# Kernel tuning notes

Hardware: AMD Instinct MI355X
Metric: run time of the kernel (lower is better)

## Reference

```python
import jax, jax.numpy as jnp
import numpy as np

N_NODES = 40000
N_EDGES = 640000
D = 128
BN_EPS = 1e-5


def setup_inputs() -> dict:
    key = jax.random.key(0)
    ks = jax.random.split(key, 8)
    h = jax.random.normal(ks[0], (N_NODES, D), dtype=jnp.float32)
    snorm_n = jax.random.uniform(ks[1], (N_NODES, 1), dtype=jnp.float32)
    W_self = jax.random.normal(ks[2], (D, D), dtype=jnp.float32) * 0.05
    W_neigh = jax.random.normal(ks[3], (D, D), dtype=jnp.float32) * 0.05
    b = jax.random.normal(ks[4], (D,), dtype=jnp.float32) * 0.05
    gamma = jnp.ones((D,), dtype=jnp.float32)
    beta = jnp.zeros((D,), dtype=jnp.float32)
    src = jax.random.randint(ks[5], (N_EDGES,), 0, N_NODES, dtype=jnp.int32)
    dst = jax.random.randint(ks[6], (N_EDGES,), 0, N_NODES, dtype=jnp.int32)
    return {"h": h, "snorm_n": snorm_n, "W_self": W_self, "W_neigh": W_neigh,
            "b": b, "gamma": gamma, "beta": beta, "src": src, "dst": dst}


def reference(h, snorm_n, W_self, W_neigh, b, gamma, beta, src, dst):
    h_in = h
    # --- SAGEConv (mean aggregator): mean over in-neighbors (src -> dst) ---
    msg = h[src]                                   # [E, D] irregular gather
    agg = jax.ops.segment_sum(msg, dst, num_segments=N_NODES)  # [N, D]
    deg = jax.ops.segment_sum(jnp.ones((N_EDGES,), h.dtype), dst,
                              num_segments=N_NODES)            # [N]
    h_neigh = agg / jnp.maximum(deg, 1.0)[:, None]
    out = h @ W_self + h_neigh @ W_neigh + b       # fc_self + fc_neigh + bias
    out = jax.nn.relu(out)                         # activation
    # --- graph norm ---
    out = out * snorm_n
    # --- batch norm (training-style batch statistics over nodes) ---
    mean = jnp.mean(out, axis=0)
    var = jnp.var(out, axis=0)
    out = (out - mean) * jax.lax.rsqrt(var + BN_EPS) * gamma + beta
    # --- residual ---
    return h_in + out
```

## Files before the change

kernel.cpp:

```cpp
#include <hip/hip_runtime.h>
#include <hip/hip_bf16.h>

constexpr int N_NODES = 40000;
constexpr int N_EDGES = 640000;
constexpr int D = 128;
constexpr float BN_EPS = 1e-5f;
constexpr int SCAN_BLOCKS = 157;

typedef __attribute__((ext_vector_type(8))) short short8;
typedef __attribute__((ext_vector_type(4))) float f32x4;

static_assert(N_EDGES == N_NODES * D / 8, "hist_cvt fusion assumes equal ranges");

__device__ __forceinline__ unsigned bf16_rne(float f) {
    unsigned b = __float_as_uint(f);
    return (b + 0x7FFFu + ((b >> 16) & 1u)) >> 16;
}
__device__ __forceinline__ float bflo(unsigned w) { return __uint_as_float(w << 16); }
__device__ __forceinline__ float bfhi(unsigned w) { return __uint_as_float(w & 0xFFFF0000u); }

__global__ void hist_cvt_kernel(const int* __restrict__ dst,
                                int* __restrict__ deg_i,
                                const float4* __restrict__ h4,
                                uint4* __restrict__ hb4,
                                const float* __restrict__ Wself,
                                const float* __restrict__ Wneigh,
                                uint4* __restrict__ wfrag) {
    int e = blockIdx.x * blockDim.x + threadIdx.x;
    if (e >= N_EDGES) return;
    atomicAdd(&deg_i[dst[e]], 1);
    float4 a = h4[2 * e];
    float4 b = h4[2 * e + 1];
    uint4 o;
    o.x = bf16_rne(a.x) | (bf16_rne(a.y) << 16);
    o.y = bf16_rne(a.z) | (bf16_rne(a.w) << 16);
    o.z = bf16_rne(b.x) | (bf16_rne(b.y) << 16);
    o.w = bf16_rne(b.z) | (bf16_rne(b.w) << 16);
    hb4[e] = o;

    if (e < 4096) {
        int G = e;
        int l = G & 63;
        int tile = G >> 6;
        int kg = l >> 4;
        int n = l & 15;
        int ct = tile >> 3;
        int kt = tile & 7;
        int k0 = kt * 32 + kg * 8;
        int col = ct * 16 + n;
        unsigned w[8];
        #pragma unroll
        for (int j = 0; j < 8; j++) {
            int k = k0 + j;
            float v = (k < D) ? Wself[(size_t)k * D + col]
                              : Wneigh[(size_t)(k - D) * D + col];
            w[j] = bf16_rne(v);
        }
        uint4 ow;
        ow.x = w[0] | (w[1] << 16);
        ow.y = w[2] | (w[3] << 16);
        ow.z = w[4] | (w[5] << 16);
        ow.w = w[6] | (w[7] << 16);
        wfrag[G] = ow;
    }
}

__global__ __launch_bounds__(256) void scan1_kernel(const int* __restrict__ deg_i,
                                                    int* __restrict__ partials) {
    __shared__ int sh[256];
    int t = threadIdx.x;
    int i = blockIdx.x * 256 + t;
    sh[t] = (i < N_NODES) ? deg_i[i] : 0;
    __syncthreads();
    for (int off = 128; off >= 1; off >>= 1) {
        if (t < off) sh[t] += sh[t + off];
        __syncthreads();
    }
    if (t == 0) partials[blockIdx.x] = sh[0];
}

__global__ __launch_bounds__(256) void scan23_kernel(const int* __restrict__ deg_i,
                                                     const int* __restrict__ partials,
                                                     int* __restrict__ row_start) {
    __shared__ int sh[256];
    __shared__ int offs;
    int t = threadIdx.x;
    int b = blockIdx.x;
    sh[t] = (t < b) ? partials[t] : 0;
    __syncthreads();
    for (int off = 128; off >= 1; off >>= 1) {
        if (t < off) sh[t] += sh[t + off];
        __syncthreads();
    }
    if (t == 0) offs = sh[0];
    __syncthreads();
    int i = b * 256 + t;
    int v = (i < N_NODES) ? deg_i[i] : 0;
    sh[t] = v;
    __syncthreads();
    for (int off = 1; off < 256; off <<= 1) {
        int u = (t >= off) ? sh[t - off] : 0;
        __syncthreads();
        sh[t] += u;
        __syncthreads();
    }
    if (i < N_NODES) row_start[i] = sh[t] - v + offs;
    if (b == SCAN_BLOCKS - 1 && t == 255) row_start[N_NODES] = sh[255] + offs;
}

__global__ void fill_kernel(const int* __restrict__ src,
                            const int* __restrict__ dst,
                            const int* __restrict__ row_start,
                            int* __restrict__ cursor,
                            int* __restrict__ esrc) {
    int e = blockIdx.x * blockDim.x + threadIdx.x;
    if (e >= N_EDGES) return;
    int t = dst[e];
    int p = atomicAdd(&cursor[t], 1);
    esrc[row_start[t] + p] = src[e];
}

__global__ __launch_bounds__(256) void gather_kernel(
        const uint4* __restrict__ hb4,
        const int* __restrict__ row_start,
        const int* __restrict__ esrc,
        uint4* __restrict__ hnb4) {
    int node = (blockIdx.x * blockDim.x + threadIdx.x) >> 6;
    int lane = threadIdx.x & 63;
    if (node >= N_NODES) return;
    int g  = lane & 15;
    int es = lane >> 4;
    int s0 = row_start[node];
    int s1 = row_start[node + 1];
    float acc[8] = {0.f, 0.f, 0.f, 0.f, 0.f, 0.f, 0.f, 0.f};
    for (int j = s0 + es; j < s1; j += 4) {
        int a = esrc[j];
        uint4 v = hb4[(size_t)a * 16 + g];
        acc[0] += bflo(v.x); acc[1] += bfhi(v.x);
        acc[2] += bflo(v.y); acc[3] += bfhi(v.y);
        acc[4] += bflo(v.z); acc[5] += bfhi(v.z);
        acc[6] += bflo(v.w); acc[7] += bfhi(v.w);
    }
    #pragma unroll
    for (int i = 0; i < 8; i++) {
        acc[i] += __shfl_xor(acc[i], 16);
        acc[i] += __shfl_xor(acc[i], 32);
    }
    if (es == 0) {
        int len = s1 - s0;
        float rd = 1.0f / (float)(len > 1 ? len : 1);
        uint4 o;
        o.x = bf16_rne(acc[0] * rd) | (bf16_rne(acc[1] * rd) << 16);
        o.y = bf16_rne(acc[2] * rd) | (bf16_rne(acc[3] * rd) << 16);
        o.z = bf16_rne(acc[4] * rd) | (bf16_rne(acc[5] * rd) << 16);
        o.w = bf16_rne(acc[6] * rd) | (bf16_rne(acc[7] * rd) << 16);
        hnb4[(size_t)node * 16 + g] = o;
    }
}

__global__ __launch_bounds__(256) void gemm_mfma_kernel(
        const uint4* __restrict__ hb4,
        const uint4* __restrict__ hnb4,
        const uint4* __restrict__ wfrag,
        const float* __restrict__ snorm,
        const float* __restrict__ bias,
        float* __restrict__ pre,
        float* __restrict__ sums,
        float* __restrict__ sumsq) {
    __shared__ uint4 ldsW[2048];
    __shared__ float sums_l[64];
    __shared__ float sumsq_l[64];

    int t = threadIdx.x;
    int lane = t & 63;
    int wid = t >> 6;
    int n = lane & 15;
    int kg = lane >> 4;
    int rowtile = blockIdx.x >> 1;
    int cbt = blockIdx.x & 1;
    int cb = cbt * 64;
    int row_base = rowtile * 64 + wid * 16;
    int row = row_base + n;

    if (t < 64) { sums_l[t] = 0.f; sumsq_l[t] = 0.f; }

    short8 a[8];
    #pragma unroll
    for (int kt = 0; kt < 4; kt++) {
        uint4 v = hb4[(size_t)row * 16 + kt * 4 + kg];
        a[kt] = __builtin_bit_cast(short8, v);
    }
    #pragma unroll
    for (int kt = 0; kt < 4; kt++) {
        uint4 v = hnb4[(size_t)row * 16 + kt * 4 + kg];
        a[4 + kt] = __builtin_bit_cast(short8, v);
    }

    #pragma unroll
    for (int i = 0; i < 8; i++) {
        int g = i * 256 + t;
        ldsW[g] = wfrag[cbt * 2048 + g];
    }
    __syncthreads();

    f32x4 acc[4];
    #pragma unroll
    for (int lt = 0; lt < 4; lt++) acc[lt] = (f32x4){0.f, 0.f, 0.f, 0.f};

    #pragma unroll
    for (int lt = 0; lt < 4; lt++) {
        #pragma unroll
        for (int kt = 0; kt < 8; kt++) {
            short8 b = __builtin_bit_cast(short8, ldsW[(lt * 8 + kt) * 64 + lane]);
            acc[lt] = __builtin_amdgcn_mfma_f32_16x16x32_bf16(a[kt], b, acc[lt], 0, 0, 0);
        }
    }

    float snv[4];
    #pragma unroll
    for (int r = 0; r < 4; r++) snv[r] = snorm[row_base + kg * 4 + r];

    #pragma unroll
    for (int lt = 0; lt < 4; lt++) {
        int col = cb + lt * 16 + n;
        float bb = bias[col];
        float csum = 0.f, csq = 0.f;
        #pragma unroll
        for (int r = 0; r < 4; r++) {
            int rr = row_base + kg * 4 + r;
            float v = acc[lt][r] + bb;
            v = fmaxf(v, 0.f);
            v *= snv[r];
            pre[(size_t)rr * D + col] = v;
            csum += v;
            csq += v * v;
        }
        csum += __shfl_xor(csum, 16); csq += __shfl_xor(csq, 16);
        csum += __shfl_xor(csum, 32); csq += __shfl_xor(csq, 32);
        if (kg == 0) {
            atomicAdd(&sums_l[lt * 16 + n], csum);
            atomicAdd(&sumsq_l[lt * 16 + n], csq);
        }
    }
    __syncthreads();
    if (t < 64) {
        atomicAdd(&sums[cb + t], sums_l[t]);
        atomicAdd(&sumsq[cb + t], sumsq_l[t]);
    }
}

__global__ void final_kernel(const float4* __restrict__ h4,
                             const float4* __restrict__ sums4,
                             const float4* __restrict__ sumsq4,
                             const float4* __restrict__ gamma4,
                             const float4* __restrict__ beta4,
                             float4* __restrict__ out4) {
    int idx = blockIdx.x * blockDim.x + threadIdx.x;
    int total = N_NODES * D / 4;
    if (idx >= total) return;
    int d4 = idx & 31;
    float4 s  = sums4[d4];
    float4 sq = sumsq4[d4];
    float4 g  = gamma4[d4];
    float4 bt = beta4[d4];
    const float invN = 1.0f / (float)N_NODES;
    float4 hv = h4[idx];
    float4 ov = out4[idx];
    float m, var, sc;
    m = s.x * invN; var = sq.x * invN - m * m; sc = g.x * rsqrtf(var + BN_EPS);
    ov.x = hv.x + (ov.x - m) * sc + bt.x;
    m = s.y * invN; var = sq.y * invN - m * m; sc = g.y * rsqrtf(var + BN_EPS);
    ov.y = hv.y + (ov.y - m) * sc + bt.y;
    m = s.z * invN; var = sq.z * invN - m * m; sc = g.z * rsqrtf(var + BN_EPS);
    ov.z = hv.z + (ov.z - m) * sc + bt.z;
    m = s.w * invN; var = sq.w * invN - m * m; sc = g.w * rsqrtf(var + BN_EPS);
    ov.w = hv.w + (ov.w - m) * sc + bt.w;
    out4[idx] = ov;
}

extern "C" void kernel_launch(void* const* d_in, const int* in_sizes, int n_in,
                              void* d_out, int out_size, void* d_ws, size_t ws_size,
                              hipStream_t stream) {
    const float* h      = (const float*)d_in[0];
    const float* snorm  = (const float*)d_in[1];
    const float* Wself  = (const float*)d_in[2];
    const float* Wneigh = (const float*)d_in[3];
    const float* bias   = (const float*)d_in[4];
    const float* gamma  = (const float*)d_in[5];
    const float* beta   = (const float*)d_in[6];
    const int*   src    = (const int*)d_in[7];
    const int*   dst    = (const int*)d_in[8];
    float* out = (float*)d_out;

    int*   deg_i     = (int*)d_ws;
    int*   cursor    = deg_i + N_NODES;
    float* sums      = (float*)(cursor + N_NODES);
    float* sumsq     = sums + D;
    int*   row_start = (int*)(sumsq + D);
    int*   partials  = row_start + (N_NODES + 1);
    int*   esrc      = partials + 160;
    size_t off       = (size_t)((char*)(esrc + N_EDGES) - (char*)d_ws);
    off = (off + 15) & ~(size_t)15;
    uint4* wfrag = (uint4*)((char*)d_ws + off);
    uint4* hb4   = wfrag + 4096;
    uint4* hnb4  = hb4 + N_NODES * (D / 8);

    size_t zero_bytes = (size_t)(2 * N_NODES + 2 * D) * sizeof(float);
    hipMemsetAsync(d_ws, 0, zero_bytes, stream);

    hist_cvt_kernel<<<N_EDGES / 256, 256, 0, stream>>>(
        dst, deg_i, (const float4*)h, hb4, Wself, Wneigh, wfrag);
    scan1_kernel<<<SCAN_BLOCKS, 256, 0, stream>>>(deg_i, partials);
    scan23_kernel<<<SCAN_BLOCKS, 256, 0, stream>>>(deg_i, partials, row_start);
    fill_kernel<<<N_EDGES / 256, 256, 0, stream>>>(src, dst, row_start, cursor, esrc);
    gather_kernel<<<N_NODES / 4, 256, 0, stream>>>(hb4, row_start, esrc, hnb4);
    gemm_mfma_kernel<<<(N_NODES / 64) * 2, 256, 0, stream>>>(
        hb4, hnb4, wfrag, snorm, bias, out, sums, sumsq);
    final_kernel<<<(N_NODES * D / 4) / 256, 256, 0, stream>>>(
        (const float4*)h, (const float4*)sums, (const float4*)sumsq,
        (const float4*)gamma, (const float4*)beta, (float4*)out);
}
```

Baseline: 207.8 us.

## Fuse all stages into one persistent cooperative kernel with grid syncs

Replaces the memset and seven separate kernel launches with one cooperative mega-kernel of 512 blocks. Stages run as grid-stride loops separated by grid.sync(): zeroing, histogram and bf16 convert, scan, CSR fill, gather, MFMA GEMM with stats, and final BN. The aim is to remove launch gaps and per-kernel tail effects. In exchange, every stage runs on a fixed grid of 512 blocks, and each grid barrier costs time and stalls the whole device. The GEMM stage also reloads weight fragments into LDS whenever a block's column half changes.

New measurement: 632.3 us. 3.04x slower.

```diff
diff --git a/kernel.cpp b/kernel.cpp
--- a/kernel.cpp
+++ b/kernel.cpp
@@ -1,16 +1,21 @@
 #include <hip/hip_runtime.h>
 #include <hip/hip_bf16.h>
+#include <hip/hip_cooperative_groups.h>
+
+namespace cg = cooperative_groups;
 
 constexpr int N_NODES = 40000;
 constexpr int N_EDGES = 640000;
 constexpr int D = 128;
 constexpr float BN_EPS = 1e-5f;
 constexpr int SCAN_BLOCKS = 157;
+constexpr int GRID = 512;
+constexpr int NTHREADS = GRID * 256;
 
 typedef __attribute__((ext_vector_type(8))) short short8;
 typedef __attribute__((ext_vector_type(4))) float f32x4;
 
-static_assert(N_EDGES == N_NODES * D / 8, "hist_cvt fusion assumes equal ranges");
+static_assert(N_EDGES == N_NODES * D / 8, "phase-1 fusion assumes equal ranges");
 
 __device__ __forceinline__ unsigned bf16_rne(float f) {
     unsigned b = __float_as_uint(f);
@@ -19,33 +24,59 @@
 __device__ __forceinline__ float bflo(unsigned w) { return __uint_as_float(w << 16); }
 __device__ __forceinline__ float bfhi(unsigned w) { return __uint_as_float(w & 0xFFFF0000u); }
 
-__global__ void hist_cvt_kernel(const int* __restrict__ dst,
-                                int* __restrict__ deg_i,
-                                const float4* __restrict__ h4,
-                                uint4* __restrict__ hb4,
-                                const float* __restrict__ Wself,
-                                const float* __restrict__ Wneigh,
-                                uint4* __restrict__ wfrag) {
-    int e = blockIdx.x * blockDim.x + threadIdx.x;
-    if (e >= N_EDGES) return;
-    atomicAdd(&deg_i[dst[e]], 1);
-    float4 a = h4[2 * e];
-    float4 b = h4[2 * e + 1];
-    uint4 o;
-    o.x = bf16_rne(a.x) | (bf16_rne(a.y) << 16);
-    o.y = bf16_rne(a.z) | (bf16_rne(a.w) << 16);
-    o.z = bf16_rne(b.x) | (bf16_rne(b.y) << 16);
-    o.w = bf16_rne(b.z) | (bf16_rne(b.w) << 16);
-    hb4[e] = o;
-
-    if (e < 4096) {
-        int G = e;
+__global__ __launch_bounds__(256) void mega_kernel(
+        const int* __restrict__ dst,
+        const int* __restrict__ src,
+        const float4* __restrict__ h4,
+        const float* __restrict__ snorm,
+        const float* __restrict__ Wself,
+        const float* __restrict__ Wneigh,
+        const float* __restrict__ bias,
+        const float4* __restrict__ gamma4,
+        const float4* __restrict__ beta4,
+        float* __restrict__ out,
+        int* __restrict__ deg_i,
+        int* __restrict__ cursor,
+        float* __restrict__ sums,
+        float* __restrict__ sumsq,
+        int* __restrict__ row_start,
+        int* __restrict__ partials,
+        int* __restrict__ esrc,
+        uint4* __restrict__ wfrag,
+        uint4* __restrict__ hb4,
+        uint4* __restrict__ hnb4) {
+    cg::grid_group grid = cg::this_grid();
+    __shared__ uint4 ldsW[2048];
+    __shared__ int sh[256];
+    __shared__ int offs_sh;
+    __shared__ float sums_l[D];
+    __shared__ float sumsq_l[D];
+
+    const int t = threadIdx.x;
+    const int b = blockIdx.x;
+    const int gtid = b * 256 + t;
+
+    for (int i = gtid; i < 2 * N_NODES; i += NTHREADS) deg_i[i] = 0;
+    if (gtid < 2 * D) sums[gtid] = 0.f;
+    grid.sync();
+
+    for (int e = gtid; e < N_EDGES; e += NTHREADS) {
+        atomicAdd(&deg_i[dst[e]], 1);
+        float4 a = h4[2 * e];
+        float4 bb = h4[2 * e + 1];
+        uint4 o;
+        o.x = bf16_rne(a.x) | (bf16_rne(a.y) << 16);
+        o.y = bf16_rne(a.z) | (bf16_rne(a.w) << 16);
+        o.z = bf16_rne(bb.x) | (bf16_rne(bb.y) << 16);
+        o.w = bf16_rne(bb.z) | (bf16_rne(bb.w) << 16);
+        hb4[e] = o;
+    }
+    if (gtid < 4096) {
+        int G = gtid;
         int l = G & 63;
         int tile = G >> 6;
-        int kg = l >> 4;
-        int n = l & 15;
-        int ct = tile >> 3;
-        int kt = tile & 7;
+        int kg = l >> 4, n = l & 15;
+        int ct = tile >> 3, kt = tile & 7;
         int k0 = kt * 32 + kg * 8;
         int col = ct * 16 + n;
         unsigned w[8];
@@ -63,233 +94,211 @@
         ow.w = w[6] | (w[7] << 16);
         wfrag[G] = ow;
     }
-}
-
-__global__ __launch_bounds__(256) void scan1_kernel(const int* __restrict__ deg_i,
-                                                    int* __restrict__ partials) {
-    __shared__ int sh[256];
-    int t = threadIdx.x;
-    int i = blockIdx.x * 256 + t;
-    sh[t] = (i < N_NODES) ? deg_i[i] : 0;
-    __syncthreads();
-    for (int off = 128; off >= 1; off >>= 1) {
-        if (t < off) sh[t] += sh[t + off];
-        __syncthreads();
-    }
-    if (t == 0) partials[blockIdx.x] = sh[0];
-}
-
-__global__ __launch_bounds__(256) void scan23_kernel(const int* __restrict__ deg_i,
-                                                     const int* __restrict__ partials,
-                                                     int* __restrict__ row_start) {
-    __shared__ int sh[256];
-    __shared__ int offs;
-    int t = threadIdx.x;
-    int b = blockIdx.x;
-    sh[t] = (t < b) ? partials[t] : 0;
-    __syncthreads();
-    for (int off = 128; off >= 1; off >>= 1) {
-        if (t < off) sh[t] += sh[t + off];
-        __syncthreads();
-    }
-    if (t == 0) offs = sh[0];
-    __syncthreads();
-    int i = b * 256 + t;
-    int v = (i < N_NODES) ? deg_i[i] : 0;
-    sh[t] = v;
-    __syncthreads();
-    for (int off = 1; off < 256; off <<= 1) {
-        int u = (t >= off) ? sh[t - off] : 0;
-        __syncthreads();
-        sh[t] += u;
-        __syncthreads();
-    }
-    if (i < N_NODES) row_start[i] = sh[t] - v + offs;
-    if (b == SCAN_BLOCKS - 1 && t == 255) row_start[N_NODES] = sh[255] + offs;
-}
-
-__global__ void fill_kernel(const int* __restrict__ src,
-                            const int* __restrict__ dst,
-                            const int* __restrict__ row_start,
-                            int* __restrict__ cursor,
-                            int* __restrict__ esrc) {
-    int e = blockIdx.x * blockDim.x + threadIdx.x;
-    if (e >= N_EDGES) return;
-    int t = dst[e];
-    int p = atomicAdd(&cursor[t], 1);
-    esrc[row_start[t] + p] = src[e];
-}
-
-__global__ __launch_bounds__(256) void gather_kernel(
-        const uint4* __restrict__ hb4,
-        const int* __restrict__ row_start,
-        const int* __restrict__ esrc,
-        uint4* __restrict__ hnb4) {
-    int node = (blockIdx.x * blockDim.x + threadIdx.x) >> 6;
-    int lane = threadIdx.x & 63;
-    if (node >= N_NODES) return;
-    int g  = lane & 15;
-    int es = lane >> 4;
-    int s0 = row_start[node];
-    int s1 = row_start[node + 1];
-    float acc[8] = {0.f, 0.f, 0.f, 0.f, 0.f, 0.f, 0.f, 0.f};
-    for (int j = s0 + es; j < s1; j += 4) {
-        int a = esrc[j];
-        uint4 v = hb4[(size_t)a * 16 + g];
-        acc[0] += bflo(v.x); acc[1] += bfhi(v.x);
-        acc[2] += bflo(v.y); acc[3] += bfhi(v.y);
-        acc[4] += bflo(v.z); acc[5] += bfhi(v.z);
-        acc[6] += bflo(v.w); acc[7] += bfhi(v.w);
-    }
-    #pragma unroll
-    for (int i = 0; i < 8; i++) {
-        acc[i] += __shfl_xor(acc[i], 16);
-        acc[i] += __shfl_xor(acc[i], 32);
-    }
-    if (es == 0) {
-        int len = s1 - s0;
-        float rd = 1.0f / (float)(len > 1 ? len : 1);
-        uint4 o;
-        o.x = bf16_rne(acc[0] * rd) | (bf16_rne(acc[1] * rd) << 16);
-        o.y = bf16_rne(acc[2] * rd) | (bf16_rne(acc[3] * rd) << 16);
-        o.z = bf16_rne(acc[4] * rd) | (bf16_rne(acc[5] * rd) << 16);
-        o.w = bf16_rne(acc[6] * rd) | (bf16_rne(acc[7] * rd) << 16);
-        hnb4[(size_t)node * 16 + g] = o;
-    }
-}
-
-__global__ __launch_bounds__(256) void gemm_mfma_kernel(
-        const uint4* __restrict__ hb4,
-        const uint4* __restrict__ hnb4,
-        const uint4* __restrict__ wfrag,
-        const float* __restrict__ snorm,
-        const float* __restrict__ bias,
-        float* __restrict__ pre,
-        float* __restrict__ sums,
-        float* __restrict__ sumsq) {
-    __shared__ uint4 ldsW[2048];
-    __shared__ float sums_l[64];
-    __shared__ float sumsq_l[64];
-
-    int t = threadIdx.x;
-    int lane = t & 63;
-    int wid = t >> 6;
-    int n = lane & 15;
-    int kg = lane >> 4;
-    int rowtile = blockIdx.x >> 1;
-    int cbt = blockIdx.x & 1;
-    int cb = cbt * 64;
-    int row_base = rowtile * 64 + wid * 16;
-    int row = row_base + n;
-
-    if (t < 64) { sums_l[t] = 0.f; sumsq_l[t] = 0.f; }
-
-    short8 a[8];
-    #pragma unroll
-    for (int kt = 0; kt < 4; kt++) {
-        uint4 v = hb4[(size_t)row * 16 + kt * 4 + kg];
-        a[kt] = __builtin_bit_cast(short8, v);
-    }
-    #pragma unroll
-    for (int kt = 0; kt < 4; kt++) {
-        uint4 v = hnb4[(size_t)row * 16 + kt * 4 + kg];
-        a[4 + kt] = __builtin_bit_cast(short8, v);
-    }
-
-    #pragma unroll
-    for (int i = 0; i < 8; i++) {
-        int g = i * 256 + t;
-        ldsW[g] = wfrag[cbt * 2048 + g];
-    }
-    __syncthreads();
-
-    f32x4 acc[4];
-    #pragma unroll
-    for (int lt = 0; lt < 4; lt++) acc[lt] = (f32x4){0.f, 0.f, 0.f, 0.f};
-
-    #pragma unroll
-    for (int lt = 0; lt < 4; lt++) {
-        #pragma unroll
-        for (int kt = 0; kt < 8; kt++) {
-            short8 b = __builtin_bit_cast(short8, ldsW[(lt * 8 + kt) * 64 + lane]);
-            acc[lt] = __builtin_amdgcn_mfma_f32_16x16x32_bf16(a[kt], b, acc[lt], 0, 0, 0);
-        }
-    }
-
-    float snv[4];
-    #pragma unroll
-    for (int r = 0; r < 4; r++) snv[r] = snorm[row_base + kg * 4 + r];
-
-    #pragma unroll
-    for (int lt = 0; lt < 4; lt++) {
-        int col = cb + lt * 16 + n;
-        float bb = bias[col];
-        float csum = 0.f, csq = 0.f;
-        #pragma unroll
-        for (int r = 0; r < 4; r++) {
-            int rr = row_base + kg * 4 + r;
-            float v = acc[lt][r] + bb;
-            v = fmaxf(v, 0.f);
-            v *= snv[r];
-            pre[(size_t)rr * D + col] = v;
-            csum += v;
-            csq += v * v;
-        }
-        csum += __shfl_xor(csum, 16); csq += __shfl_xor(csq, 16);
-        csum += __shfl_xor(csum, 32); csq += __shfl_xor(csq, 32);
-        if (kg == 0) {
-            atomicAdd(&sums_l[lt * 16 + n], csum);
-            atomicAdd(&sumsq_l[lt * 16 + n], csq);
-        }
-    }
-    __syncthreads();
-    if (t < 64) {
-        atomicAdd(&sums[cb + t], sums_l[t]);
-        atomicAdd(&sumsq[cb + t], sumsq_l[t]);
-    }
-}
-
-__global__ void final_kernel(const float4* __restrict__ h4,
-                             const float4* __restrict__ sums4,
-                             const float4* __restrict__ sumsq4,
-                             const float4* __restrict__ gamma4,
-                             const float4* __restrict__ beta4,
-                             float4* __restrict__ out4) {
-    int idx = blockIdx.x * blockDim.x + threadIdx.x;
-    int total = N_NODES * D / 4;
-    if (idx >= total) return;
-    int d4 = idx & 31;
-    float4 s  = sums4[d4];
-    float4 sq = sumsq4[d4];
-    float4 g  = gamma4[d4];
-    float4 bt = beta4[d4];
-    const float invN = 1.0f / (float)N_NODES;
-    float4 hv = h4[idx];
-    float4 ov = out4[idx];
-    float m, var, sc;
-    m = s.x * invN; var = sq.x * invN - m * m; sc = g.x * rsqrtf(var + BN_EPS);
-    ov.x = hv.x + (ov.x - m) * sc + bt.x;
-    m = s.y * invN; var = sq.y * invN - m * m; sc = g.y * rsqrtf(var + BN_EPS);
-    ov.y = hv.y + (ov.y - m) * sc + bt.y;
-    m = s.z * invN; var = sq.z * invN - m * m; sc = g.z * rsqrtf(var + BN_EPS);
-    ov.z = hv.z + (ov.z - m) * sc + bt.z;
-    m = s.w * invN; var = sq.w * invN - m * m; sc = g.w * rsqrtf(var + BN_EPS);
-    ov.w = hv.w + (ov.w - m) * sc + bt.w;
-    out4[idx] = ov;
+    grid.sync();
+
+    if (b < SCAN_BLOCKS) {
+        int i = b * 256 + t;
+        sh[t] = (i < N_NODES) ? deg_i[i] : 0;
+        __syncthreads();
+        for (int off = 128; off >= 1; off >>= 1) {
+            if (t < off) sh[t] += sh[t + off];
+            __syncthreads();
+        }
+        if (t == 0) partials[b] = sh[0];
+    }
+    grid.sync();
+
+    if (b < SCAN_BLOCKS) {
+        sh[t] = (t < b) ? partials[t] : 0;
+        __syncthreads();
+        for (int off = 128; off >= 1; off >>= 1) {
+            if (t < off) sh[t] += sh[t + off];
+            __syncthreads();
+        }
+        if (t == 0) offs_sh = sh[0];
+        __syncthreads();
+        int offs = offs_sh;
+        int i = b * 256 + t;
+        int v = (i < N_NODES) ? deg_i[i] : 0;
+        __syncthreads();
+        sh[t] = v;
+        __syncthreads();
+        for (int off = 1; off < 256; off <<= 1) {
+            int u = (t >= off) ? sh[t - off] : 0;
+            __syncthreads();
+            sh[t] += u;
+            __syncthreads();
+        }
+        if (i < N_NODES) row_start[i] = sh[t] - v + offs;
+        if (b == SCAN_BLOCKS - 1 && t == 255) row_start[N_NODES] = sh[255] + offs;
+    }
+    grid.sync();
+
+    for (int e = gtid; e < N_EDGES; e += NTHREADS) {
+        int tt = dst[e];
+        int p = atomicAdd(&cursor[tt], 1);
+        esrc[row_start[tt] + p] = src[e];
+    }
+    grid.sync();
+
+    {
+        int lane = t & 63;
+        int g = lane & 15;
+        int es = lane >> 4;
+        int wglob = b * 4 + (t >> 6);
+        for (int node = wglob; node < N_NODES; node += GRID * 4) {
+            int s0 = row_start[node];
+            int s1 = row_start[node + 1];
+            float acc[8] = {0.f, 0.f, 0.f, 0.f, 0.f, 0.f, 0.f, 0.f};
+            for (int j = s0 + es; j < s1; j += 4) {
+                int a = esrc[j];
+                uint4 v = hb4[(size_t)a * 16 + g];
+                acc[0] += bflo(v.x); acc[1] += bfhi(v.x);
+                acc[2] += bflo(v.y); acc[3] += bfhi(v.y);
+                acc[4] += bflo(v.z); acc[5] += bfhi(v.z);
+                acc[6] += bflo(v.w); acc[7] += bfhi(v.w);
+            }
+            #pragma unroll
+            for (int i = 0; i < 8; i++) {
+                acc[i] += __shfl_xor(acc[i], 16);
+                acc[i] += __shfl_xor(acc[i], 32);
+            }
+            if (es == 0) {
+                int len = s1 - s0;
+                float rd = 1.0f / (float)(len > 1 ? len : 1);
+                uint4 o;
+                o.x = bf16_rne(acc[0] * rd) | (bf16_rne(acc[1] * rd) << 16);
+                o.y = bf16_rne(acc[2] * rd) | (bf16_rne(acc[3] * rd) << 16);
+                o.z = bf16_rne(acc[4] * rd) | (bf16_rne(acc[5] * rd) << 16);
+                o.w = bf16_rne(acc[6] * rd) | (bf16_rne(acc[7] * rd) << 16);
+                hnb4[(size_t)node * 16 + g] = o;
+            }
+        }
+    }
+    grid.sync();
+
+    {
+        if (t < D) { sums_l[t] = 0.f; sumsq_l[t] = 0.f; }
+        int lane = t & 63;
+        int wid = t >> 6;
+        int n = lane & 15;
+        int kg = lane >> 4;
+        int cur_cbt = -1;
+        for (int idx = b; idx < 1250; idx += GRID) {
+            int cbt = (idx >= 625) ? 1 : 0;
+            int rowtile = idx - cbt * 625;
+            if (cbt != cur_cbt) {
+                __syncthreads();
+                #pragma unroll
+                for (int i = 0; i < 8; i++) {
+                    int g = i * 256 + t;
+                    ldsW[g] = wfrag[cbt * 2048 + g];
+                }
+                __syncthreads();
+                cur_cbt = cbt;
+            }
+            int cb = cbt * 64;
+            int row_base = rowtile * 64 + wid * 16;
+            int row = row_base + n;
+
+            short8 a[8];
+            #pragma unroll
+            for (int kt = 0; kt < 4; kt++) {
+                uint4 v = hb4[(size_t)row * 16 + kt * 4 + kg];
+                a[kt] = __builtin_bit_cast(short8, v);
+            }
+            #pragma unroll
+            for (int kt = 0; kt < 4; kt++) {
+                uint4 v = hnb4[(size_t)row * 16 + kt * 4 + kg];
+                a[4 + kt] = __builtin_bit_cast(short8, v);
+            }
+
+            f32x4 acc[4];
+            #pragma unroll
+            for (int lt = 0; lt < 4; lt++) acc[lt] = (f32x4){0.f, 0.f, 0.f, 0.f};
+            #pragma unroll
+            for (int lt = 0; lt < 4; lt++) {
+                #pragma unroll
+                for (int kt = 0; kt < 8; kt++) {
+                    short8 bb = __builtin_bit_cast(short8, ldsW[(lt * 8 + kt) * 64 + lane]);
+                    acc[lt] = __builtin_amdgcn_mfma_f32_16x16x32_bf16(a[kt], bb, acc[lt], 0, 0, 0);
+                }
+            }
+
+            float snv[4];
+            #pragma unroll
+            for (int r = 0; r < 4; r++) snv[r] = snorm[row_base + kg * 4 + r];
+
+            #pragma unroll
+            for (int lt = 0; lt < 4; lt++) {
+                int col = cb + lt * 16 + n;
+                float bbias = bias[col];
+                float csum = 0.f, csq = 0.f;
+                #pragma unroll
+                for (int r = 0; r < 4; r++) {
+                    int rr = row_base + kg * 4 + r;
+                    float v = acc[lt][r] + bbias;
+                    v = fmaxf(v, 0.f);
+                    v *= snv[r];
+                    out[(size_t)rr * D + col] = v;
+                    csum += v;
+                    csq += v * v;
+                }
+                csum += __shfl_xor(csum, 16); csq += __shfl_xor(csq, 16);
+                csum += __shfl_xor(csum, 32); csq += __shfl_xor(csq, 32);
+                if (kg == 0) {
+                    atomicAdd(&sums_l[col], csum);
+                    atomicAdd(&sumsq_l[col], csq);
+                }
+            }
+        }
+        __syncthreads();
+        if (t < D) {
+            atomicAdd(&sums[t], sums_l[t]);
+            atomicAdd(&sumsq[t], sumsq_l[t]);
+        }
+    }
+    grid.sync();
+
+    {
+        const float invN = 1.0f / (float)N_NODES;
+        const float4* sums4 = (const float4*)sums;
+        const float4* sumsq4 = (const float4*)sumsq;
+        float4* out4 = (float4*)out;
+        for (int idx = gtid; idx < N_NODES * D / 4; idx += NTHREADS) {
+            int d4 = idx & 31;
+            float4 s = sums4[d4];
+            float4 sq = sumsq4[d4];
+            float4 g = gamma4[d4];
+            float4 bt = beta4[d4];
+            float4 hv = h4[idx];
+            float4 ov = out4[idx];
+            float m, var, sc;
+            m = s.x * invN; var = sq.x * invN - m * m; sc = g.x * rsqrtf(var + BN_EPS);
+            ov.x = hv.x + (ov.x - m) * sc + bt.x;
+            m = s.y * invN; var = sq.y * invN - m * m; sc = g.y * rsqrtf(var + BN_EPS);
+            ov.y = hv.y + (ov.y - m) * sc + bt.y;
+            m = s.z * invN; var = sq.z * invN - m * m; sc = g.z * rsqrtf(var + BN_EPS);
+            ov.z = hv.z + (ov.z - m) * sc + bt.z;
+            m = s.w * invN; var = sq.w * invN - m * m; sc = g.w * rsqrtf(var + BN_EPS);
+            ov.w = hv.w + (ov.w - m) * sc + bt.w;
+            out4[idx] = ov;
+        }
+    }
 }
 
 extern "C" void kernel_launch(void* const* d_in, const int* in_sizes, int n_in,
                               void* d_out, int out_size, void* d_ws, size_t ws_size,
                               hipStream_t stream) {
-    const float* h      = (const float*)d_in[0];
-    const float* snorm  = (const float*)d_in[1];
-    const float* Wself  = (const float*)d_in[2];
-    const float* Wneigh = (const float*)d_in[3];
-    const float* bias   = (const float*)d_in[4];
-    const float* gamma  = (const float*)d_in[5];
-    const float* beta   = (const float*)d_in[6];
-    const int*   src    = (const int*)d_in[7];
-    const int*   dst    = (const int*)d_in[8];
+    const float4* h4    = (const float4*)d_in[0];
+    const float*  snorm = (const float*)d_in[1];
+    const float*  Wself = (const float*)d_in[2];
+    const float*  Wneigh= (const float*)d_in[3];
+    const float*  bias  = (const float*)d_in[4];
+    const float4* gamma4= (const float4*)d_in[5];
+    const float4* beta4 = (const float4*)d_in[6];
+    const int*    src   = (const int*)d_in[7];
+    const int*    dst   = (const int*)d_in[8];
     float* out = (float*)d_out;
 
     int*   deg_i     = (int*)d_ws;
@@ -305,18 +314,13 @@
     uint4* hb4   = wfrag + 4096;
     uint4* hnb4  = hb4 + N_NODES * (D / 8);
 
-    size_t zero_bytes = (size_t)(2 * N_NODES + 2 * D) * sizeof(float);
-    hipMemsetAsync(d_ws, 0, zero_bytes, stream);
-
-    hist_cvt_kernel<<<N_EDGES / 256, 256, 0, stream>>>(
-        dst, deg_i, (const float4*)h, hb4, Wself, Wneigh, wfrag);
-    scan1_kernel<<<SCAN_BLOCKS, 256, 0, stream>>>(deg_i, partials);
-    scan23_kernel<<<SCAN_BLOCKS, 256, 0, stream>>>(deg_i, partials, row_start);
-    fill_kernel<<<N_EDGES / 256, 256, 0, stream>>>(src, dst, row_start, cursor, esrc);
-    gather_kernel<<<N_NODES / 4, 256, 0, stream>>>(hb4, row_start, esrc, hnb4);
-    gemm_mfma_kernel<<<(N_NODES / 64) * 2, 256, 0, stream>>>(
-        hb4, hnb4, wfrag, snorm, bias, out, sums, sumsq);
-    final_kernel<<<(N_NODES * D / 4) / 256, 256, 0, stream>>>(
-        (const float4*)h, (const float4*)sums, (const float4*)sumsq,
-        (const float4*)gamma, (const float4*)beta, (float4*)out);
+    void* args[] = {
+        (void*)&dst, (void*)&src, (void*)&h4, (void*)&snorm, (void*)&Wself,
+        (void*)&Wneigh, (void*)&bias, (void*)&gamma4, (void*)&beta4,
+        (void*)&out, (void*)&deg_i, (void*)&cursor, (void*)&sums,
+        (void*)&sumsq, (void*)&row_start, (void*)&partials, (void*)&esrc,
+        (void*)&wfrag, (void*)&hb4, (void*)&hnb4,
+    };
+    hipLaunchCooperativeKernel((const void*)mega_kernel, dim3(GRID), dim3(256),
+                               args, 0, stream);
 }
```
